# Kernel optimization log

Hardware: AMD Instinct MI355X
Metric: run time of the kernel (lower is better)

## Reference

```python
import jax, jax.numpy as jnp
import numpy as np

B, S = 4, 1024          # 4 prefill sequences of length 1024 (cu_seqlens equal-length)
D_MODEL = 2048
N_HEADS = 32
N_KV_HEADS = 8
HEAD_DIM = D_MODEL // N_HEADS          # 64
GROUPS = N_HEADS // N_KV_HEADS         # 4
ROPE_THETA = 10000.0
SCALE = HEAD_DIM ** -0.5


def setup_inputs() -> dict:
    key = jax.random.key(0)
    ks = jax.random.split(key, 6)
    T = B * S
    hidden_states = jax.random.normal(ks[0], (T, D_MODEL), jnp.float32)
    # rotary tables: positions restart per sequence (prefill)
    pos = jnp.tile(jnp.arange(S, dtype=jnp.float32), B)            # [T]
    inv_freq = 1.0 / (ROPE_THETA ** (jnp.arange(0, HEAD_DIM, 2, dtype=jnp.float32) / HEAD_DIM))
    freqs = pos[:, None] * inv_freq[None, :]                        # [T, HEAD_DIM/2]
    cos, sin = jnp.cos(freqs), jnp.sin(freqs)
    std = D_MODEL ** -0.5
    Wq = jax.random.normal(ks[1], (D_MODEL, N_HEADS * HEAD_DIM), jnp.float32) * std
    Wk = jax.random.normal(ks[2], (D_MODEL, N_KV_HEADS * HEAD_DIM), jnp.float32) * std
    Wv = jax.random.normal(ks[3], (D_MODEL, N_KV_HEADS * HEAD_DIM), jnp.float32) * std
    Wo = jax.random.normal(ks[4], (N_HEADS * HEAD_DIM, D_MODEL), jnp.float32) * std
    return {"hidden_states": hidden_states, "cos": cos, "sin": sin,
            "Wq": Wq, "Wk": Wk, "Wv": Wv, "Wo": Wo}


def _rope(x, cos, sin):
    # NeoX-style rotary: x [T, H, D], cos/sin [T, D/2]
    half = x.shape[-1] // 2
    x1, x2 = x[..., :half], x[..., half:]
    c, s = cos[:, None, :], sin[:, None, :]
    return jnp.concatenate([x1 * c - x2 * s, x2 * c + x1 * s], axis=-1)


def reference(hidden_states, cos, sin, Wq, Wk, Wv, Wo):
    T = hidden_states.shape[0]
    q = (hidden_states @ Wq).reshape(T, N_HEADS, HEAD_DIM)
    k = (hidden_states @ Wk).reshape(T, N_KV_HEADS, HEAD_DIM)
    v = (hidden_states @ Wv).reshape(T, N_KV_HEADS, HEAD_DIM)
    q = _rope(q, cos, sin)
    k = _rope(k, cos, sin)
    # equal-length varlen prefill -> [B, S, H, D]
    q = q.reshape(B, S, N_HEADS, HEAD_DIM)
    k = jnp.repeat(k.reshape(B, S, N_KV_HEADS, HEAD_DIM), GROUPS, axis=2)  # GQA expand
    v = jnp.repeat(v.reshape(B, S, N_KV_HEADS, HEAD_DIM), GROUPS, axis=2)
    scores = jnp.einsum("bqhd,bkhd->bhqk", q, k) * SCALE
    causal = jnp.tril(jnp.ones((S, S), dtype=bool))
    scores = jnp.where(causal[None, None], scores, jnp.finfo(scores.dtype).min)
    probs = jax.nn.softmax(scores, axis=-1)
    attn = jnp.einsum("bhqk,bkhd->bqhd", probs, v).reshape(T, N_HEADS * HEAD_DIM)
    return attn @ Wo
```

## Files before the change

kernel.cpp:

```cpp
#include <hip/hip_runtime.h>
#include <type_traits>


typedef __bf16 bf16x8 __attribute__((ext_vector_type(8)));
typedef __bf16 bf16x4 __attribute__((ext_vector_type(4)));
typedef float f32x4 __attribute__((ext_vector_type(4)));
typedef unsigned short u16;
typedef unsigned int u32;

#define DEVI __device__ __forceinline__

DEVI u16 f2bf(float f) {
  u32 u = __builtin_bit_cast(u32, f);
  u += 0x7FFF + ((u >> 16) & 1);
  return (u16)(u >> 16);
}

DEVI void ld16_lds(const void* g, void* l) {
  __builtin_amdgcn_global_load_lds((const __attribute__((address_space(1))) u32*)g,
                                   (__attribute__((address_space(3))) u32*)l, 16, 0, 0);
}

template <int N> DEVI void waitvm() {
  if constexpr (N == 0) asm volatile("s_waitcnt vmcnt(0)" ::: "memory");
  else if constexpr (N == 6) asm volatile("s_waitcnt vmcnt(6)" ::: "memory");
  else if constexpr (N == 7) asm volatile("s_waitcnt vmcnt(7)" ::: "memory");
  else if constexpr (N == 8) asm volatile("s_waitcnt vmcnt(8)" ::: "memory");
  else if constexpr (N == 10) asm volatile("s_waitcnt vmcnt(10)" ::: "memory");
  else static_assert(N == 0, "unsupported vmcnt");
}
DEVI void lgkm0() {
  asm volatile("s_waitcnt lgkmcnt(0)" ::: "memory");
  __builtin_amdgcn_sched_barrier(0);
}
DEVI void barrier() { __builtin_amdgcn_s_barrier(); }

__global__ __launch_bounds__(256) void prep(const float* __restrict__ hs, u16* __restrict__ hsB,
                                            const float* __restrict__ Wq, const float* __restrict__ Wk,
                                            const float* __restrict__ Wv, const float* __restrict__ Wo,
                                            u16* __restrict__ wqkvT, u16* __restrict__ woT,
                                            float qscale) {
  int b = blockIdx.x;
  if (b < 8192) {
    int i = b * 256 + threadIdx.x;
    float4 v = ((const float4*)hs)[i];
    ushort4 o;
    o.x = f2bf(v.x); o.y = f2bf(v.y); o.z = f2bf(v.z); o.w = f2bf(v.w);
    ((ushort4*)hsB)[i] = o;
    return;
  }
  b -= 8192;
  const float* src; u16* dst; int R, C, bx, by; float sc = 1.0f;
  if (b < 4096)      { src = Wq; dst = wqkvT;                         R = 2048; C = 2048; bx = b & 63; by = b >> 6; sc = qscale; }
  else if (b < 5120) { b -= 4096; src = Wk; dst = wqkvT + (size_t)2048 * 2048; R = 2048; C = 512; bx = b & 15; by = b >> 4; }
  else if (b < 6144) { b -= 5120; src = Wv; dst = wqkvT + (size_t)2560 * 2048; R = 2048; C = 512; bx = b & 15; by = b >> 4; }
  else               { b -= 6144; src = Wo; dst = woT;                R = 2048; C = 2048; bx = b & 63; by = b >> 6; }
  __shared__ float tile[32][33];
  int c0 = bx * 32, r0 = by * 32;
  int tx = threadIdx.x & 31, ty = threadIdx.x >> 5;
#pragma unroll
  for (int i = 0; i < 32; i += 8)
    tile[ty + i][tx] = src[(size_t)(r0 + ty + i) * C + (c0 + tx)];
  __syncthreads();
#pragma unroll
  for (int i = 0; i < 32; i += 8)
    dst[(size_t)(c0 + ty + i) * R + (r0 + tx)] = f2bf(tile[tx][ty + i] * sc);
}

template <typename OutT, int BN>
__global__ __launch_bounds__(256, 2) void gemm2(const u16* __restrict__ A,
                                                const u16* __restrict__ BT,
                                                OutT* __restrict__ C, int M, int N, int K) {
  constexpr int NF = BN / 32;
  constexpr int NH = NF / 2;
  constexpr int HW = BN / 2;
  constexpr int SW = HW / 2;
  constexpr int LB0 = BN / 64;
  constexpr int VMW = 4 + 2 * LB0;
  constexpr int VMP = 4 + LB0;
  __shared__ u16 As[2][128 * 64];
  __shared__ u16 Bs[2][BN * 64];
  const int tid = threadIdx.x;
  const int lane = tid & 63, wave = tid >> 6;
  const int quad = lane >> 4, l16 = lane & 15;

  const int nwg = gridDim.x * gridDim.y;
  const int bid = blockIdx.y * gridDim.x + blockIdx.x;
  const int swz = (bid & 7) * (nwg >> 3) + (bid >> 3);
  const int m0 = (swz / gridDim.x) * 128, n0 = (swz % gridDim.x) * BN;
  const int wr = wave >> 1, wc = wave & 1;

  f32x4 acc[4][NF] = {};

  auto stA = [&](int t) {
    u16* D = &As[t & 1][0];
    const u16* G = A + (size_t)m0 * K + t * 64;
#pragma unroll
    for (int i = 0; i < 4; ++i) {
      int id = i * 256 + tid, row = id >> 3, ch = id & 7;
      ld16_lds(G + (size_t)row * K + (ch ^ (row & 7)) * 8, D + id * 8);
    }
  };
  auto stB = [&](int t, int h) {
    u16* D = &Bs[t & 1][h * HW * 64];
    const u16* G = BT + (size_t)(n0 + h * HW) * K + t * 64;
#pragma unroll
    for (int i = 0; i < LB0; ++i) {
      int id = i * 256 + tid, row = id >> 3, ch = id & 7;
      ld16_lds(G + (size_t)row * K + (ch ^ (row & 7)) * 8, D + id * 8);
    }
  };

  bf16x8 af[4][2], bv0[NH][2], bv1[NH][2];
  auto ldA = [&](int d) {
#pragma unroll
    for (int i = 0; i < 4; ++i)
#pragma unroll
      for (int ks = 0; ks < 2; ++ks) {
        int r = wr * 64 + i * 16 + l16;
        af[i][ks] = *(const bf16x8*)&As[d][r * 64 + (((ks * 4 + quad) ^ (r & 7)) * 8)];
      }
  };
  auto ldB = [&](bf16x8 (&bv)[NH][2], int half, int d) {
#pragma unroll
    for (int j = 0; j < NH; ++j)
#pragma unroll
      for (int ks = 0; ks < 2; ++ks) {
        int rb = half * HW + wc * SW + j * 16 + l16;
        bv[j][ks] = *(const bf16x8*)&Bs[d][rb * 64 + (((ks * 4 + quad) ^ (rb & 7)) * 8)];
      }
  };
  auto mm = [&](bf16x8 (&bv)[NH][2], int jo) {
    __builtin_amdgcn_s_setprio(1);
#pragma unroll
    for (int i = 0; i < 4; ++i)
#pragma unroll
      for (int j = 0; j < NH; ++j)
#pragma unroll
        for (int ks = 0; ks < 2; ++ks)
          acc[i][jo + j] =
              __builtin_amdgcn_mfma_f32_16x16x32_bf16(af[i][ks], bv[j][ks], acc[i][jo + j], 0, 0, 0);
    __builtin_amdgcn_s_setprio(0);
  };

  const int NT = K / 64;

  stA(0); stB(0, 0); stB(0, 1);
  stA(1); stB(1, 0);
  waitvm<VMP>();
  barrier();

#pragma unroll 2
  for (int t = 0; t < NT; ++t) {
    const int buf = t & 1;
    const bool deep = (t + 2 < NT);
    ldA(buf); ldB(bv0, 0, buf);
    if (t + 1 < NT) stB(t + 1, 1);
    barrier(); lgkm0();
    mm(bv0, 0);
    if (deep) waitvm<VMW>(); else waitvm<0>();
    barrier();
    ldB(bv1, 1, buf);
    if (deep) { stA(t + 2); stB(t + 2, 0); }
    barrier(); lgkm0();
    mm(bv1, NH);
    if (deep) waitvm<VMW>(); else waitvm<0>();
    barrier();
  }

#pragma unroll
  for (int i = 0; i < 4; ++i) {
    int row = m0 + wr * 64 + i * 16 + quad * 4;
#pragma unroll
    for (int j = 0; j < NF; ++j) {
      int half = j / NH, jj = j % NH;
      int col = n0 + half * HW + wc * SW + jj * 16 + l16;
#pragma unroll
      for (int r = 0; r < 4; ++r) {
        size_t off = (size_t)(row + r) * N + col;
        if constexpr (sizeof(OutT) == 2) C[off] = f2bf(acc[i][j][r]);
        else C[off] = acc[i][j][r];
      }
    }
  }
}

__global__ __launch_bounds__(256) void rope_vkt(u16* __restrict__ qkv,
                                                u16* __restrict__ vkt,
                                                const float* __restrict__ cs,
                                                const float* __restrict__ sn) {
  const int kt = blockIdx.x, h = blockIdx.y, b = blockIdx.z;
  const int tid = threadIdx.x;
  const size_t tok0 = (size_t)b * 1024 + (size_t)kt * 128;

  {
    const int r = tid >> 1, hf = tid & 1;
    const size_t t = tok0 + r;
    const float* cr = cs + t * 32;
    const float* sr = sn + t * 32;
    u16* qrow = qkv + t * 3072 + h * 64;
    u16* krow = qkv + t * 3072 + 2048 + h * 64;
#pragma unroll
    for (int gg = 0; gg < 2; ++gg) {
      const int g = hf * 2 + gg;
      float cv[8], sv[8];
#pragma unroll
      for (int e = 0; e < 8; ++e) { cv[e] = cr[g * 8 + e]; sv[e] = sr[g * 8 + e]; }
      {
        bf16x8 a = *(bf16x8*)&qrow[g * 8];
        bf16x8 b2 = *(bf16x8*)&qrow[g * 8 + 32];
#pragma unroll
        for (int e = 0; e < 8; ++e) {
          float x1 = (float)a[e], x2 = (float)b2[e];
          a[e] = (__bf16)(x1 * cv[e] - x2 * sv[e]);
          b2[e] = (__bf16)(x2 * cv[e] + x1 * sv[e]);
        }
        *(bf16x8*)&qrow[g * 8] = a;
        *(bf16x8*)&qrow[g * 8 + 32] = b2;
      }
      if (h < 8) {
        bf16x8 a = *(bf16x8*)&krow[g * 8];
        bf16x8 b2 = *(bf16x8*)&krow[g * 8 + 32];
#pragma unroll
        for (int e = 0; e < 8; ++e) {
          float x1 = (float)a[e], x2 = (float)b2[e];
          a[e] = (__bf16)(x1 * cv[e] - x2 * sv[e]);
          b2[e] = (__bf16)(x2 * cv[e] + x1 * sv[e]);
        }
        *(bf16x8*)&krow[g * 8] = a;
        *(bf16x8*)&krow[g * 8 + 32] = b2;
      }
    }
  }
  if (h >= 8) return;

  __shared__ u16 Vn[128 * 64];
  const u16* src = qkv + tok0 * 3072 + 2560 + h * 64;
  {
    int tok = tid >> 1, hf = tid & 1;
    const uint4* s4 = (const uint4*)(src + (size_t)tok * 3072 + hf * 32);
    uint4* d4 = (uint4*)&Vn[tok * 64 + hf * 32];
#pragma unroll
    for (int j = 0; j < 4; j++) d4[j] = s4[j];
  }
  __syncthreads();
  u16* img = vkt + ((((size_t)b * 8 + h) * 8 + kt) << 13);
#pragma unroll
  for (int i = 0; i < 4; i++) {
    int c = tid * 4 + i;
    int dd = c >> 4, chsw = c & 15;
    int ch = chsw ^ (dd & 15);
    u16 tmp[8];
#pragma unroll
    for (int p = 0; p < 8; p++) {
      int col = ch * 8 + p;
      int g = col >> 5, kl = col & 31;
      int kph = ((kl >> 2) & 1) * 16 + ((kl >> 4) & 1) * 8 + ((kl >> 3) & 1) * 4 + (kl & 3);
      tmp[p] = Vn[(g * 32 + kph) * 64 + dd];
    }
    *(uint4*)&img[c * 8] = *(const uint4*)tmp;
  }
}

__global__ __launch_bounds__(256, 2) void flash_attn(const u16* __restrict__ qkv,
                                                     const u16* __restrict__ vkt,
                                                     u16* __restrict__ attn) {
  __shared__ u16 Ks[2][128 * 64];
  __shared__ u16 VT[2][64 * 128];

  const int tid = threadIdx.x;
  const int lane = tid & 63, wave = tid >> 6;
  const int quad = lane >> 4, l16 = lane & 15;
  const int qtA = blockIdx.x, qtB = 7 - blockIdx.x;
  const int h = blockIdx.y, b = blockIdx.z, kvh = h >> 2;
  const size_t tokBase = (size_t)b * 1024;
  const int qcol = h * 64, kcol = 2048 + kvh * 64;
  const int srow = tid >> 3, spc = tid & 7, ssc = spc ^ (srow & 7);

  auto stageK = [&](const u16* gbase, u16* L) {
#pragma unroll
    for (int i = 0; i < 4; i++)
      ld16_lds(gbase + (size_t)(srow + i * 32) * 3072 + ssc * 8, &L[tid * 8 + i * 2048]);
  };
  const u16* vimg = vkt + (((size_t)b * 8 + kvh) << 16);
  auto stageV = [&](int kt, u16* L) {
    const u16* g = vimg + ((size_t)kt << 13);
#pragma unroll
    for (int i = 0; i < 4; i++)
      ld16_lds(g + i * 2048 + tid * 8, &L[tid * 8 + i * 2048]);
  };

  stageK(qkv + (tokBase + qtA * 128) * 3072 + qcol, Ks[0]);
  stageK(qkv + (tokBase + qtB * 128) * 3072 + qcol, Ks[1]);
  __syncthreads();
  bf16x8 qfA[2][2], qfB[2][2];
#pragma unroll
  for (int nq = 0; nq < 2; nq++) {
    int qrow = wave * 32 + nq * 16 + l16;
#pragma unroll
    for (int ks = 0; ks < 2; ks++) {
      int c = (ks * 4 + quad) ^ (qrow & 7);
      qfA[nq][ks] = *(const bf16x8*)&Ks[0][qrow * 64 + c * 8];
      qfB[nq][ks] = *(const bf16x8*)&Ks[1][qrow * 64 + c * 8];
    }
  }
  __syncthreads();

  float lA[2] = {0.f, 0.f}, lB[2] = {0.f, 0.f};
  f32x4 oA[4][2] = {}, oB[4][2] = {};

  auto proc = [&](const bf16x8 (&kf)[2][2], const bf16x8 (&va)[4], const bf16x8 (&qf)[2][2],
                  f32x4 (&o)[4][2], float (&lacc)[2], bool msk, int c) {
    f32x4 s[2][2] = {};
    __builtin_amdgcn_s_setprio(1);
#pragma unroll
    for (int mkl = 0; mkl < 2; mkl++)
#pragma unroll
      for (int ks = 0; ks < 2; ks++) {
        s[0][mkl] = __builtin_amdgcn_mfma_f32_16x16x32_bf16(kf[mkl][ks], qf[0][ks], s[0][mkl], 0, 0, 0);
        s[1][mkl] = __builtin_amdgcn_mfma_f32_16x16x32_bf16(kf[mkl][ks], qf[1][ks], s[1][mkl], 0, 0, 0);
      }
    __builtin_amdgcn_s_setprio(0);
    if (msk) {
#pragma unroll
      for (int nq = 0; nq < 2; nq++) {
        int q = wave * 32 + nq * 16 + l16;
#pragma unroll
        for (int mkl = 0; mkl < 2; mkl++)
#pragma unroll
          for (int r = 0; r < 4; r++)
            if ((c * 2 + mkl) * 16 + quad * 4 + r > q) s[nq][mkl][r] = -3e38f;
      }
    }
    bf16x8 pf[2];
#pragma unroll
    for (int nq = 0; nq < 2; nq++) {
      float a0 = 0.f;
#pragma unroll
      for (int mkl = 0; mkl < 2; mkl++)
#pragma unroll
        for (int r = 0; r < 4; r++) {
          float p = __builtin_amdgcn_exp2f(s[nq][mkl][r]);
          s[nq][mkl][r] = p;
          a0 += p;
        }
      lacc[nq] += a0;
      pf[nq][0] = (__bf16)s[nq][0][0]; pf[nq][1] = (__bf16)s[nq][0][1];
      pf[nq][2] = (__bf16)s[nq][0][2]; pf[nq][3] = (__bf16)s[nq][0][3];
      pf[nq][4] = (__bf16)s[nq][1][0]; pf[nq][5] = (__bf16)s[nq][1][1];
      pf[nq][6] = (__bf16)s[nq][1][2]; pf[nq][7] = (__bf16)s[nq][1][3];
    }
    __builtin_amdgcn_s_setprio(1);
#pragma unroll
    for (int md = 0; md < 4; md++) {
      o[md][0] = __builtin_amdgcn_mfma_f32_16x16x32_bf16(va[md], pf[0], o[md][0], 0, 0, 0);
      o[md][1] = __builtin_amdgcn_mfma_f32_16x16x32_bf16(va[md], pf[1], o[md][1], 0, 0, 0);
    }
    __builtin_amdgcn_s_setprio(0);
  };

  stageK(qkv + tokBase * 3072 + kcol, Ks[0]);
  stageV(0, VT[0]);

  for (int kt = 0; kt <= qtB; kt++) {
    const int cur = kt & 1;
    __syncthreads();
    if (kt < qtB) {
      stageK(qkv + (tokBase + (kt + 1) * 128) * 3072 + kcol, Ks[1 - cur]);
      stageV(kt + 1, VT[1 - cur]);
    }
    const bool doA = (kt <= qtA), mA = (kt == qtA), mB = (kt == qtB);
    const u16* K = Ks[cur];
    const u16* V = VT[cur];
#pragma unroll
    for (int c = 0; c < 4; c++) {
      bf16x8 kf[2][2];
#pragma unroll
      for (int mkl = 0; mkl < 2; mkl++) {
        int krow = (c * 2 + mkl) * 16 + l16;
#pragma unroll
        for (int ks = 0; ks < 2; ks++)
          kf[mkl][ks] = *(const bf16x8*)&K[krow * 64 + ((ks * 4 + quad) ^ (krow & 7)) * 8];
      }
      bf16x8 va[4];
#pragma unroll
      for (int md = 0; md < 4; md++) {
        int dd = md * 16 + l16;
        va[md] = *(const bf16x8*)&V[dd * 128 + ((c * 4 + quad) ^ l16) * 8];
      }
      proc(kf, va, qfB, oB, lB, mB, c);
      if (doA) proc(kf, va, qfA, oA, lA, mA, c);
    }
  }

  auto epilogue = [&](const f32x4 (&o)[4][2], const float (&lacc)[2], int qt_tile) {
#pragma unroll
    for (int nq = 0; nq < 2; nq++) {
      float l = lacc[nq];
      l += __shfl_xor(l, 16);
      l += __shfl_xor(l, 32);
      float inv = 1.0f / l;
      int t = qt_tile * 128 + wave * 32 + nq * 16 + l16;
      size_t rowOff = (tokBase + t) * 2048 + qcol;
#pragma unroll
      for (int md = 0; md < 4; md++) {
        bf16x4 w;
        w[0] = (__bf16)(o[md][nq][0] * inv);
        w[1] = (__bf16)(o[md][nq][1] * inv);
        w[2] = (__bf16)(o[md][nq][2] * inv);
        w[3] = (__bf16)(o[md][nq][3] * inv);
        *(bf16x4*)&attn[rowOff + md * 16 + quad * 4] = w;
      }
    }
  };
  epilogue(oB, lB, qtB);
  epilogue(oA, lA, qtA);
}

extern "C" void kernel_launch(void* const* d_in, const int* in_sizes, int n_in,
                              void* d_out, int out_size, void* d_ws, size_t ws_size,
                              hipStream_t stream) {
  const float* hs = (const float*)d_in[0];
  const float* cs = (const float*)d_in[1];
  const float* sn = (const float*)d_in[2];
  const float* Wq = (const float*)d_in[3];
  const float* Wk = (const float*)d_in[4];
  const float* Wv = (const float*)d_in[5];
  const float* Wo = (const float*)d_in[6];
  float* out = (float*)d_out;

  char* ws = (char*)d_ws;
  u16* hsB   = (u16*)(ws);
  u16* vkt   = (u16*)(ws);
  u16* wqkvT = (u16*)(ws + 16777216);
  u16* woT   = (u16*)(ws + 29360128);
  u16* qkv   = (u16*)(ws + 37748736);
  u16* attnB = (u16*)(ws + 62914560);

  const float QSCALE = 0.18033688011112042f;

  prep<<<18432, 256, 0, stream>>>(hs, hsB, Wq, Wk, Wv, Wo, wqkvT, woT, QSCALE);

  gemm2<u16, 192><<<dim3(16, 32), 256, 0, stream>>>(hsB, wqkvT, qkv, 4096, 3072, 2048);
  rope_vkt<<<dim3(8, 32, 4), 256, 0, stream>>>(qkv, vkt, cs, sn);
  flash_attn<<<dim3(4, 32, 4), 256, 0, stream>>>(qkv, vkt, attnB);
  gemm2<float, 128><<<dim3(16, 32), 256, 0, stream>>>(attnB, woT, out, 4096, 2048, 2048);
}
```

Before: 253.7 us.

## Restructure GEMM main loop with register double-buffering and one barrier per step

Replaces the split-half GEMM loop, which had four barriers per k-tile, with a schedule that issues the whole A and B tile load two steps ahead. The fragments for the next tile are read from LDS into registers while the MFMAs for the current tile run, so each k-step needs only one barrier. The cost is a second copy of the A fragments in registers, which raises VGPR pressure. It also adds a full vmcnt(0) wait every iteration, which can expose global-load latency that the earlier partial waits kept hidden.

```diff
diff --git a/kernel.cpp b/kernel.cpp
--- a/kernel.cpp
+++ b/kernel.cpp
@@ -23,8 +23,6 @@
 
 template <int N> DEVI void waitvm() {
   if constexpr (N == 0) asm volatile("s_waitcnt vmcnt(0)" ::: "memory");
-  else if constexpr (N == 6) asm volatile("s_waitcnt vmcnt(6)" ::: "memory");
-  else if constexpr (N == 7) asm volatile("s_waitcnt vmcnt(7)" ::: "memory");
   else if constexpr (N == 8) asm volatile("s_waitcnt vmcnt(8)" ::: "memory");
   else if constexpr (N == 10) asm volatile("s_waitcnt vmcnt(10)" ::: "memory");
   else static_assert(N == 0, "unsupported vmcnt");
@@ -68,7 +66,7 @@
 }
 
 template <typename OutT, int BN>
-__global__ __launch_bounds__(256, 2) void gemm2(const u16* __restrict__ A,
+__global__ __launch_bounds__(256, 2) void gemm3(const u16* __restrict__ A,
                                                 const u16* __restrict__ BT,
                                                 OutT* __restrict__ C, int M, int N, int K) {
   constexpr int NF = BN / 32;
@@ -77,7 +75,6 @@
   constexpr int SW = HW / 2;
   constexpr int LB0 = BN / 64;
   constexpr int VMW = 4 + 2 * LB0;
-  constexpr int VMP = 4 + LB0;
   __shared__ u16 As[2][128 * 64];
   __shared__ u16 Bs[2][BN * 64];
   const int tid = threadIdx.x;
@@ -92,45 +89,49 @@
 
   f32x4 acc[4][NF] = {};
 
-  auto stA = [&](int t) {
-    u16* D = &As[t & 1][0];
-    const u16* G = A + (size_t)m0 * K + t * 64;
-#pragma unroll
-    for (int i = 0; i < 4; ++i) {
-      int id = i * 256 + tid, row = id >> 3, ch = id & 7;
-      ld16_lds(G + (size_t)row * K + (ch ^ (row & 7)) * 8, D + id * 8);
-    }
-  };
-  auto stB = [&](int t, int h) {
-    u16* D = &Bs[t & 1][h * HW * 64];
-    const u16* G = BT + (size_t)(n0 + h * HW) * K + t * 64;
-#pragma unroll
-    for (int i = 0; i < LB0; ++i) {
-      int id = i * 256 + tid, row = id >> 3, ch = id & 7;
-      ld16_lds(G + (size_t)row * K + (ch ^ (row & 7)) * 8, D + id * 8);
-    }
-  };
-
-  bf16x8 af[4][2], bv0[NH][2], bv1[NH][2];
-  auto ldA = [&](int d) {
+  auto stage = [&](int t) {
+    const int buf = t & 1;
+    {
+      u16* D = &As[buf][0];
+      const u16* G = A + (size_t)m0 * K + t * 64;
+#pragma unroll
+      for (int i = 0; i < 4; ++i) {
+        int id = i * 256 + tid, row = id >> 3, ch = id & 7;
+        ld16_lds(G + (size_t)row * K + (ch ^ (row & 7)) * 8, D + id * 8);
+      }
+    }
+#pragma unroll
+    for (int h = 0; h < 2; ++h) {
+      u16* D = &Bs[buf][h * HW * 64];
+      const u16* G = BT + (size_t)(n0 + h * HW) * K + t * 64;
+#pragma unroll
+      for (int i = 0; i < LB0; ++i) {
+        int id = i * 256 + tid, row = id >> 3, ch = id & 7;
+        ld16_lds(G + (size_t)row * K + (ch ^ (row & 7)) * 8, D + id * 8);
+      }
+    }
+  };
+
+  bf16x8 af[2][4][2], b0[NH][2], b1[NH][2];
+  auto ldAF = [&](int s, int buf) {
 #pragma unroll
     for (int i = 0; i < 4; ++i)
 #pragma unroll
       for (int ks = 0; ks < 2; ++ks) {
         int r = wr * 64 + i * 16 + l16;
-        af[i][ks] = *(const bf16x8*)&As[d][r * 64 + (((ks * 4 + quad) ^ (r & 7)) * 8)];
-      }
-  };
-  auto ldB = [&](bf16x8 (&bv)[NH][2], int half, int d) {
+        af[s][i][ks] = *(const bf16x8*)&As[buf][r * 64 + (((ks * 4 + quad) ^ (r & 7)) * 8)];
+      }
+  };
+  auto ldB = [&](bf16x8 (&bv)[NH][2], int half, int buf) {
 #pragma unroll
     for (int j = 0; j < NH; ++j)
 #pragma unroll
       for (int ks = 0; ks < 2; ++ks) {
         int rb = half * HW + wc * SW + j * 16 + l16;
-        bv[j][ks] = *(const bf16x8*)&Bs[d][rb * 64 + (((ks * 4 + quad) ^ (rb & 7)) * 8)];
-      }
-  };
-  auto mm = [&](bf16x8 (&bv)[NH][2], int jo) {
+        bv[j][ks] = *(const bf16x8*)&Bs[buf][rb * 64 + (((ks * 4 + quad) ^ (rb & 7)) * 8)];
+      }
+  };
+  auto mmh = [&](int s, bf16x8 (&bv)[NH][2], int jo) {
     __builtin_amdgcn_s_setprio(1);
 #pragma unroll
     for (int i = 0; i < 4; ++i)
@@ -139,33 +140,33 @@
 #pragma unroll
         for (int ks = 0; ks < 2; ++ks)
           acc[i][jo + j] =
-              __builtin_amdgcn_mfma_f32_16x16x32_bf16(af[i][ks], bv[j][ks], acc[i][jo + j], 0, 0, 0);
+              __builtin_amdgcn_mfma_f32_16x16x32_bf16(af[s][i][ks], bv[j][ks], acc[i][jo + j], 0, 0, 0);
     __builtin_amdgcn_s_setprio(0);
   };
 
   const int NT = K / 64;
 
-  stA(0); stB(0, 0); stB(0, 1);
-  stA(1); stB(1, 0);
-  waitvm<VMP>();
+  stage(0); stage(1);
+  waitvm<VMW>();
+  barrier();
+  ldAF(0, 0); ldB(b0, 0, 0); ldB(b1, 1, 0);
+  lgkm0();
   barrier();
 
 #pragma unroll 2
   for (int t = 0; t < NT; ++t) {
-    const int buf = t & 1;
-    const bool deep = (t + 2 < NT);
-    ldA(buf); ldB(bv0, 0, buf);
-    if (t + 1 < NT) stB(t + 1, 1);
-    barrier(); lgkm0();
-    mm(bv0, 0);
-    if (deep) waitvm<VMW>(); else waitvm<0>();
-    barrier();
-    ldB(bv1, 1, buf);
-    if (deep) { stA(t + 2); stB(t + 2, 0); }
-    barrier(); lgkm0();
-    mm(bv1, NH);
-    if (deep) waitvm<VMW>(); else waitvm<0>();
-    barrier();
+    const int cur = t & 1, nxt = cur ^ 1;
+    if (t + 2 < NT) stage(t + 2);
+    if (t + 1 < NT) ldAF(nxt, nxt);
+    mmh(cur, b0, 0);
+    if (t + 1 < NT) ldB(b0, 0, nxt);
+    mmh(cur, b1, NH);
+    if (t + 1 < NT) {
+      ldB(b1, 1, nxt);
+      waitvm<0>();
+      lgkm0();
+      barrier();
+    }
   }
 
 #pragma unroll
@@ -441,8 +442,8 @@
 
   prep<<<18432, 256, 0, stream>>>(hs, hsB, Wq, Wk, Wv, Wo, wqkvT, woT, QSCALE);
 
-  gemm2<u16, 192><<<dim3(16, 32), 256, 0, stream>>>(hsB, wqkvT, qkv, 4096, 3072, 2048);
+  gemm3<u16, 192><<<dim3(16, 32), 256, 0, stream>>>(hsB, wqkvT, qkv, 4096, 3072, 2048);
   rope_vkt<<<dim3(8, 32, 4), 256, 0, stream>>>(qkv, vkt, cs, sn);
   flash_attn<<<dim3(4, 32, 4), 256, 0, stream>>>(qkv, vkt, attnB);
-  gemm2<float, 128><<<dim3(16, 32), 256, 0, stream>>>(attnB, woT, out, 4096, 2048, 2048);
-}
+  gemm3<float, 128><<<dim3(16, 32), 256, 0, stream>>>(attnB, woT, out, 4096, 2048, 2048);
+}
```

Measured after the change: 514.6 us. 2.03x slower.
